# Optimization experiments

Hardware: AMD Instinct MI355X
Metric: run time of the kernel (lower is better)

## Reference

```python
import jax, jax.numpy as jnp
import numpy as np
import itertools
jax.config.update("jax_enable_x64", True)

ND, NQ, B = 4, 3, 256          # ndrives, nqubits, batch_size
D = 2 ** NQ                     # Hilbert-space dim = 8


def _pauli_basis(nq):
    I = np.eye(2, dtype=np.complex128)
    X = np.array([[0, 1], [1, 0]], dtype=np.complex128)
    Y = np.array([[0, -1j], [1j, 0]], dtype=np.complex128)
    Z = np.array([[1, 0], [0, -1]], dtype=np.complex128)
    mats = []
    for combo in itertools.product([I, X, Y, Z], repeat=nq):
        m = np.array([[1.0 + 0j]], dtype=np.complex128)
        for s in combo:
            m = np.kron(m, s)
        mats.append(m)
    return np.stack(mats)  # [4**nq, 2**nq, 2**nq], Hermitian


def setup_inputs() -> dict:
    key = jax.random.key(0)
    k1, k2, k3 = jax.random.split(key, 3)
    paulies = jnp.asarray(_pauli_basis(NQ))          # [64, 8, 8] complex128
    L = paulies.shape[0]
    x = jax.random.normal(k1, (B, ND), dtype=jnp.float64)
    # keras 'normal' initializer ~ stddev 0.05
    kernel = 0.05 * jax.random.normal(k2, (ND, L), dtype=jnp.float64)
    bias = 0.05 * jax.random.normal(k3, (L,), dtype=jnp.float64)
    return {"x": x, "kernel": kernel, "bias": bias, "paulies": paulies}


def _probs(pw_i, paulies):
    # pw_i: [L] real pauli weights for one sample
    H = jnp.tensordot(pw_i.astype(jnp.complex128), paulies, axes=[[0], [0]])  # [D, D]
    e, v = jnp.linalg.eigh(H)                      # Hermitian eigendecomp
    expe = jnp.exp(-1j * e)                        # [D]
    # amp_j = sum_s conj(v)[0,s] * exp(-i e_s) * v[j,s]  (evolution of |0>)
    amp = jnp.einsum('s,js->j', jnp.conj(v[0, :]) * expe, v)  # [D]
    return amp.real ** 2 + amp.imag ** 2           # P, [D] float64


def reference(x, kernel, bias, paulies):
    pw = x @ kernel + bias                         # [B, L]
    f = lambda p: _probs(p, paulies)
    P = jax.vmap(f)(pw)                            # [B, D]
    # per-sample Jacobian dP/d(pauli_weights): [B, D, L]
    g = jax.vmap(jax.jacrev(f))(pw)
    oneoverp = 1.0 / P                             # [B, D]
    # chain rule: pw = x @ kernel + bias  =>  dP/dkernel[i,p,j,k] = x[i,j] * g[i,p,k]
    p_k = jnp.einsum('ij,ipk->ipjk', x, g)         # [B, D, ND, L]
    I_k = jnp.einsum('ipjk,iplm,ip->ijklm', p_k, p_k, oneoverp)  # [B, ND, L, ND, L]
    I_b = jnp.einsum('ipj,ipk,ip->ijk', g, g, oneoverp)          # [B, L, L]
    return (I_k, I_b)
```

## Files before the change

### kernel.cpp

```cpp
#include <hip/hip_runtime.h>
#include <math.h>

typedef float f4_t __attribute__((ext_vector_type(4)));

#define NTERM 20
#define TROW  9
#define TMAT  (TROW * 8)

__device__ __forceinline__ double rdin(const void* p, int idx, bool isdbl) {
  return isdbl ? ((const double*)p)[idx] : (double)((const float*)p)[idx];
}

__global__ __launch_bounds__(256) void fi_all(
    const void* __restrict__ xv,
    const void* __restrict__ kv,
    const void* __restrict__ bv,
    float* __restrict__ out, int Bn)
{
  const int i    = blockIdx.x;
  const int t    = threadIdx.x;
  const int wv   = t >> 6;
  const int tl   = t & 63;
  const int swv  = i & 3;
  const bool solver = (wv == swv);

  __shared__ float  pw[64];
  __shared__ float2 Zl[8][8];
  __shared__ float  invfact[48];
  __shared__ float2 Tall[NTERM * TMAT];
  __shared__ float2 Rl[NTERM][8];
  __shared__ float2 Ql[8][8][8];
  __shared__ float  ampre[8], ampim[8], invPs[8];
  __shared__ __align__(16) float gk_km[64][8];
  __shared__ __align__(16) float hk_t[8][68];

  const bool isdbl =
      (__ballot(!(fabsf(((const float*)xv)[tl]) < 1e6f)) != 0ull);

  if (solver) {
    float acc = (float)rdin(bv, tl, isdbl);
    #pragma unroll
    for (int j = 0; j < 4; ++j)
      acc += (float)rdin(xv, i*4 + j, isdbl) * (float)rdin(kv, j*64 + tl, isdbl);
    pw[tl] = acc;
  } else if (wv == ((swv + 1) & 3) && tl < 48) {
    int n = tl;
    float f = 1.0f;
    for (int u = 2; u <= n; ++u) f *= __builtin_amdgcn_rcpf((float)u);
    invfact[n] = f;
  }
  __syncthreads();

  if (solver) {
    int r = tl >> 3, c = tl & 7;
    int m = r ^ c;
    float hre = 0.0f, him = 0.0f;
    for (int u = 0; u < 8; ++u) {
      int k = 0;
      float pr = 1.0f, pim = 0.0f;
      #pragma unroll
      for (int q = 0; q < 3; ++q) {
        int bit = 2 - q;
        int f  = (m >> bit) & 1;
        int ch = (u >> bit) & 1;
        int rb = (r >> bit) & 1;
        int d  = f ? (ch ? 2 : 1) : (ch ? 3 : 0);
        k = (k << 2) | d;
        if (d == 2) {
          float nr = rb ? -pim : pim;
          float ni = rb ?  pr  : -pr;
          pr = nr; pim = ni;
        } else if (d == 3 && rb) { pr = -pr; pim = -pim; }
      }
      float w = pw[k];
      hre += w * pr; him += w * pim;
    }
    Zl[r][c] = make_float2(him, -hre);
  }
  __syncthreads();

  if (solver) {
    const int r = tl >> 3, c = tl & 7;
    float2 Zrow[8];
    #pragma unroll
    for (int u = 0; u < 8; ++u) Zrow[u] = Zl[r][u];
    float Tre = (r == c) ? 1.0f : 0.0f;
    float Tim = 0.0f;
    Tall[r*TROW + c] = make_float2(Tre, Tim);
    #pragma unroll
    for (int j = 1; j < NTERM; ++j) {
      float cr[8], ci[8];
      #pragma unroll
      for (int u = 0; u < 8; ++u) {
        int srcl = (((u << 3) | c) << 2);
        cr[u] = __int_as_float(__builtin_amdgcn_ds_bpermute(srcl, __float_as_int(Tre)));
        ci[u] = __int_as_float(__builtin_amdgcn_ds_bpermute(srcl, __float_as_int(Tim)));
      }
      float nr = 0.0f, ni = 0.0f;
      #pragma unroll
      for (int u = 0; u < 8; ++u) {
        nr += Zrow[u].x*cr[u] - Zrow[u].y*ci[u];
        ni += Zrow[u].x*ci[u] + Zrow[u].y*cr[u];
      }
      Tre = nr; Tim = ni;
      Tall[j*TMAT + r*TROW + c] = make_float2(nr, ni);
    }
  }
  __syncthreads();

  if (t < NTERM * 8) {
    const int l = t >> 3, b = t & 7;
    float sr = 0.0f, si = 0.0f;
    for (int j = 0; j < NTERM; ++j) {
      float cf = invfact[j + l + 1];
      float2 a = Tall[j*TMAT + b*TROW];
      sr += cf * a.x; si += cf * a.y;
    }
    Rl[l][b] = make_float2(sr, si);
  }
  if (t >= 192 && t < 200) {
    const int b = t - 192;
    float ar = 0.0f, ai = 0.0f;
    for (int j = 0; j < NTERM; ++j) {
      float cf = invfact[j];
      float2 a = Tall[j*TMAT + b*TROW];
      ar += cf * a.x; ai += cf * a.y;
    }
    ampre[b] = ar; ampim[b] = ai;
    float P = ar*ar + ai*ai;
    invPs[b] = 1.0f / fmaxf(P, 1e-30f);
  }
  __syncthreads();

  {
    const int p  = t >> 5;
    const int a  = (t >> 2) & 7;
    const int b0 = (t & 3) << 1;
    float q0r = 0.f, q0i = 0.f, q1r = 0.f, q1i = 0.f;
    for (int l = 0; l < NTERM; ++l) {
      float2 T  = Tall[l*TMAT + p*TROW + a];
      f4_t  rp  = *(const f4_t*)&Rl[l][b0];
      q0r += T.x*rp.x - T.y*rp.y;  q0i += T.x*rp.y + T.y*rp.x;
      q1r += T.x*rp.z - T.y*rp.w;  q1i += T.x*rp.w + T.y*rp.z;
    }
    Ql[p][a][b0]   = make_float2(q0r, q0i);
    Ql[p][a][b0+1] = make_float2(q1r, q1i);
  }
  __syncthreads();

  {
    const int k  = t & 63;
    const int pg = t >> 6;
    const int p0 = pg << 1, p1 = p0 + 1;
    const int d0 = (k >> 4) & 3, d1 = (k >> 2) & 3, d2 = k & 3;
    const int m = ((((d0 == 1) | (d0 == 2)) ? 1 : 0) << 2)
                | ((((d1 == 1) | (d1 == 2)) ? 1 : 0) << 1)
                |  (((d2 == 1) | (d2 == 2)) ? 1 : 0);
    float S0r = 0.f, S0i = 0.f, S1r = 0.f, S1i = 0.f;
    #pragma unroll
    for (int a = 0; a < 8; ++a) {
      float pr = 1.0f, pim = 0.0f;
      const int dd[3] = {d0, d1, d2};
      #pragma unroll
      for (int q = 0; q < 3; ++q) {
        int rb = (a >> (2 - q)) & 1;
        int d = dd[q];
        if (d == 2) {
          float nr = rb ? -pim : pim;
          float ni = rb ?  pr  : -pr;
          pr = nr; pim = ni;
        } else if (d == 3 && rb) { pr = -pr; pim = -pim; }
      }
      const int b = a ^ m;
      float2 qa = Ql[p0][a][b];
      float2 qb = Ql[p1][a][b];
      S0r += pr*qa.x - pim*qa.y;  S0i += pr*qa.y + pim*qa.x;
      S1r += pr*qb.x - pim*qb.y;  S1i += pr*qb.y + pim*qb.x;
    }
    float g0 = 2.0f * (ampre[p0]*S0i - ampim[p0]*S0r);
    float g1 = 2.0f * (ampre[p1]*S1i - ampim[p1]*S1r);
    *(float2*)&gk_km[k][p0] = make_float2(g0, g1);
    hk_t[p0][k] = g0 * invPs[p0];
    hk_t[p1][k] = g1 * invPs[p1];
  }

  float sc[4];
  {
    float xl = (float)rdin(xv, i*4 + (tl >> 4), isdbl);
    #pragma unroll
    for (int jj = 0; jj < 4; ++jj)
      sc[jj] = xl * (float)rdin(xv, i*4 + jj, isdbl);
  }
  __syncthreads();

  const int m4 = (tl & 15) << 2;
  f4_t hv[8];
  #pragma unroll
  for (int p = 0; p < 8; ++p) hv[p] = *(const f4_t*)&hk_t[p][m4];

  {
    float* ok = out + (size_t)i * 65536;
    #pragma unroll
    for (int it = 0; it < 16; ++it) {
      const int k = it*4 + wv;
      const f4_t ga = *(const f4_t*)&gk_km[k][0];
      const f4_t gb = *(const f4_t*)&gk_km[k][4];
      f4_t acc = ga.x*hv[0] + ga.y*hv[1] + ga.z*hv[2] + ga.w*hv[3]
               + gb.x*hv[4] + gb.y*hv[5] + gb.z*hv[6] + gb.w*hv[7];
      #pragma unroll
      for (int jj = 0; jj < 4; ++jj) {
        f4_t vv = sc[jj] * acc;
        *(f4_t*)(ok + (size_t)jj*16384 + (size_t)k*256 + (size_t)tl*4) = vv;
      }
    }
  }

  {
    float* ob = out + (size_t)Bn * 65536 + (size_t)i * 4096;
    #pragma unroll
    for (int r = 0; r < 4; ++r) {
      const int k = r*16 + (t >> 4);
      const f4_t ga = *(const f4_t*)&gk_km[k][0];
      const f4_t gb = *(const f4_t*)&gk_km[k][4];
      f4_t acc = ga.x*hv[0] + ga.y*hv[1] + ga.z*hv[2] + ga.w*hv[3]
               + gb.x*hv[4] + gb.y*hv[5] + gb.z*hv[6] + gb.w*hv[7];
      *(f4_t*)(ob + (size_t)r*1024 + (size_t)t*4) = acc;
    }
  }
}

extern "C" void kernel_launch(void* const* d_in, const int* in_sizes, int n_in,
                              void* d_out, int out_size, void* d_ws, size_t ws_size,
                              hipStream_t stream) {
  (void)n_in; (void)d_ws; (void)ws_size; (void)out_size;
  int Bn = in_sizes[0] / 4;
  fi_all<<<Bn, 256, 0, stream>>>(d_in[0], d_in[1], d_in[2], (float*)d_out, Bn);
}
```

Measured before the change: 93.06 us.

## Split matrix power series across all four wavefronts using repeated squaring

Instead of one solver wavefront computing Z^1..Z^19 serially, every wavefront builds pw and Z redundantly in registers via cross-lane permutes. Each wavefront then jumps to its own starting power (Z^0, Z^5, Z^10, Z^15) by squaring and computes five consecutive powers. This removes two barriers and shortens the serial chain of matrix products. The inverse-factorial table becomes a constant array. Redundant work grows across wavefronts, and squaring changes float rounding slightly.

Result: faster. 91.23 us, median of 2 (-2.0%).

```diff
diff --git a/kernel.cpp b/kernel.cpp
--- a/kernel.cpp
+++ b/kernel.cpp
@@ -7,8 +7,57 @@
 #define TROW  9
 #define TMAT  (TROW * 8)
 
+__device__ const float INVFACT[48] = {
+  1.0f, 1.0f, 5.0e-1f, 1.66666666666667e-1f, 4.16666666666667e-2f,
+  8.33333333333333e-3f, 1.38888888888889e-3f, 1.98412698412698e-4f,
+  2.48015873015873e-5f, 2.75573192239859e-6f, 2.75573192239859e-7f,
+  2.50521083854417e-8f, 2.08767569878681e-9f, 1.60590438368216e-10f,
+  1.14707455977297e-11f, 7.64716373181982e-13f, 4.77947733238738e-14f,
+  2.81145725434552e-15f, 1.56192069685862e-16f, 8.22063524662433e-18f,
+  4.11031762331216e-19f, 1.95729410633913e-20f, 8.89679139245057e-22f,
+  3.86817017063068e-23f, 1.61173757109612e-24f, 6.44695028438447e-26f,
+  2.47959626322480e-27f, 9.18368986379555e-29f, 3.27988923706984e-30f,
+  1.13099628864477e-31f, 3.76998762881591e-33f, 1.21612504155352e-34f,
+  3.80039075485474e-36f, 1.15163356207720e-37f, 3.38715753552116e-39f,
+  0.f, 0.f, 0.f, 0.f, 0.f, 0.f, 0.f, 0.f, 0.f, 0.f, 0.f, 0.f, 0.f
+};
+
 __device__ __forceinline__ double rdin(const void* p, int idx, bool isdbl) {
   return isdbl ? ((const double*)p)[idx] : (double)((const float*)p)[idx];
+}
+
+__device__ __forceinline__ float bpf(int srcl, float v) {
+  return __int_as_float(__builtin_amdgcn_ds_bpermute(srcl, __float_as_int(v)));
+}
+
+__device__ __forceinline__ void gmul(float& Cr, float& Ci,
+                                     float Ar, float Ai, float Br, float Bi,
+                                     int r, int c) {
+  float nr = 0.f, ni = 0.f;
+  #pragma unroll
+  for (int u = 0; u < 8; ++u) {
+    int sa = ((r << 3) | u) << 2;
+    int sb = ((u << 3) | c) << 2;
+    float ar = bpf(sa, Ar), ai = bpf(sa, Ai);
+    float br = bpf(sb, Br), bi = bpf(sb, Bi);
+    nr += ar*br - ai*bi;
+    ni += ar*bi + ai*br;
+  }
+  Cr = nr; Ci = ni;
+}
+
+__device__ __forceinline__ void zmul(float& Cr, float& Ci,
+                                     float Br, float Bi,
+                                     const float2* Zrow, int c) {
+  float nr = 0.f, ni = 0.f;
+  #pragma unroll
+  for (int u = 0; u < 8; ++u) {
+    int sb = ((u << 3) | c) << 2;
+    float br = bpf(sb, Br), bi = bpf(sb, Bi);
+    nr += Zrow[u].x*br - Zrow[u].y*bi;
+    ni += Zrow[u].x*bi + Zrow[u].y*br;
+  }
+  Cr = nr; Ci = ni;
 }
 
 __global__ __launch_bounds__(256) void fi_all(
@@ -21,12 +70,7 @@
   const int t    = threadIdx.x;
   const int wv   = t >> 6;
   const int tl   = t & 63;
-  const int swv  = i & 3;
-  const bool solver = (wv == swv);
-
-  __shared__ float  pw[64];
-  __shared__ float2 Zl[8][8];
-  __shared__ float  invfact[48];
+
   __shared__ float2 Tall[NTERM * TMAT];
   __shared__ float2 Rl[NTERM][8];
   __shared__ float2 Ql[8][8][8];
@@ -37,27 +81,19 @@
   const bool isdbl =
       (__ballot(!(fabsf(((const float*)xv)[tl]) < 1e6f)) != 0ull);
 
-  if (solver) {
-    float acc = (float)rdin(bv, tl, isdbl);
-    #pragma unroll
-    for (int j = 0; j < 4; ++j)
-      acc += (float)rdin(xv, i*4 + j, isdbl) * (float)rdin(kv, j*64 + tl, isdbl);
-    pw[tl] = acc;
-  } else if (wv == ((swv + 1) & 3) && tl < 48) {
-    int n = tl;
-    float f = 1.0f;
-    for (int u = 2; u <= n; ++u) f *= __builtin_amdgcn_rcpf((float)u);
-    invfact[n] = f;
-  }
-  __syncthreads();
-
-  if (solver) {
-    int r = tl >> 3, c = tl & 7;
+  float pwv = (float)rdin(bv, tl, isdbl);
+  #pragma unroll
+  for (int j = 0; j < 4; ++j)
+    pwv += (float)rdin(xv, i*4 + j, isdbl) * (float)rdin(kv, j*64 + tl, isdbl);
+
+  const int r = tl >> 3, c = tl & 7;
+  float Zre, Zim;
+  {
     int m = r ^ c;
-    float hre = 0.0f, him = 0.0f;
+    float hre = 0.f, him = 0.f;
+    #pragma unroll
     for (int u = 0; u < 8; ++u) {
-      int k = 0;
-      float pr = 1.0f, pim = 0.0f;
+      int k = 0; float pr = 1.f, pim = 0.f;
       #pragma unroll
       for (int q = 0; q < 3; ++q) {
         int bit = 2 - q;
@@ -72,38 +108,48 @@
           pr = nr; pim = ni;
         } else if (d == 3 && rb) { pr = -pr; pim = -pim; }
       }
-      float w = pw[k];
+      float w = bpf(k << 2, pwv);
       hre += w * pr; him += w * pim;
     }
-    Zl[r][c] = make_float2(him, -hre);
-  }
-  __syncthreads();
-
-  if (solver) {
-    const int r = tl >> 3, c = tl & 7;
-    float2 Zrow[8];
-    #pragma unroll
-    for (int u = 0; u < 8; ++u) Zrow[u] = Zl[r][u];
-    float Tre = (r == c) ? 1.0f : 0.0f;
-    float Tim = 0.0f;
-    Tall[r*TROW + c] = make_float2(Tre, Tim);
-    #pragma unroll
-    for (int j = 1; j < NTERM; ++j) {
-      float cr[8], ci[8];
-      #pragma unroll
-      for (int u = 0; u < 8; ++u) {
-        int srcl = (((u << 3) | c) << 2);
-        cr[u] = __int_as_float(__builtin_amdgcn_ds_bpermute(srcl, __float_as_int(Tre)));
-        ci[u] = __int_as_float(__builtin_amdgcn_ds_bpermute(srcl, __float_as_int(Tim)));
-      }
-      float nr = 0.0f, ni = 0.0f;
-      #pragma unroll
-      for (int u = 0; u < 8; ++u) {
-        nr += Zrow[u].x*cr[u] - Zrow[u].y*ci[u];
-        ni += Zrow[u].x*ci[u] + Zrow[u].y*cr[u];
-      }
-      Tre = nr; Tim = ni;
-      Tall[j*TMAT + r*TROW + c] = make_float2(nr, ni);
+    Zre = him; Zim = -hre;
+  }
+
+  float2 Zrow[8];
+  #pragma unroll
+  for (int u = 0; u < 8; ++u) {
+    int s = ((r << 3) | u) << 2;
+    Zrow[u] = make_float2(bpf(s, Zre), bpf(s, Zim));
+  }
+
+  float Z2r, Z2i; zmul(Z2r, Z2i, Zre, Zim, Zrow, c);
+  if (wv == 0) {
+    Tall[0*TMAT + r*TROW + c] = make_float2((r == c) ? 1.f : 0.f, 0.f);
+    Tall[1*TMAT + r*TROW + c] = make_float2(Zre, Zim);
+    Tall[2*TMAT + r*TROW + c] = make_float2(Z2r, Z2i);
+    float cr_ = Z2r, ci_ = Z2i;
+    #pragma unroll
+    for (int s = 3; s < 5; ++s) {
+      float nr_, ni_; zmul(nr_, ni_, cr_, ci_, Zrow, c);
+      cr_ = nr_; ci_ = ni_;
+      Tall[s*TMAT + r*TROW + c] = make_float2(cr_, ci_);
+    }
+  } else {
+    float Z4r, Z4i; gmul(Z4r, Z4i, Z2r, Z2i, Z2r, Z2i, r, c);
+    float Z5r, Z5i; zmul(Z5r, Z5i, Z4r, Z4i, Zrow, c);
+    float Cr_, Ci_;
+    if (wv == 1) { Cr_ = Z5r; Ci_ = Z5i; }
+    else {
+      float Z10r, Z10i; gmul(Z10r, Z10i, Z5r, Z5i, Z5r, Z5i, r, c);
+      if (wv == 2) { Cr_ = Z10r; Ci_ = Z10i; }
+      else         { gmul(Cr_, Ci_, Z10r, Z10i, Z5r, Z5i, r, c); }
+    }
+    const int base = wv * 5;
+    Tall[base*TMAT + r*TROW + c] = make_float2(Cr_, Ci_);
+    #pragma unroll
+    for (int s = 1; s < 5; ++s) {
+      float nr_, ni_; zmul(nr_, ni_, Cr_, Ci_, Zrow, c);
+      Cr_ = nr_; Ci_ = ni_;
+      Tall[(base + s)*TMAT + r*TROW + c] = make_float2(Cr_, Ci_);
     }
   }
   __syncthreads();
@@ -111,8 +157,9 @@
   if (t < NTERM * 8) {
     const int l = t >> 3, b = t & 7;
     float sr = 0.0f, si = 0.0f;
+    #pragma unroll
     for (int j = 0; j < NTERM; ++j) {
-      float cf = invfact[j + l + 1];
+      float cf = INVFACT[j + l + 1];
       float2 a = Tall[j*TMAT + b*TROW];
       sr += cf * a.x; si += cf * a.y;
     }
@@ -121,8 +168,9 @@
   if (t >= 192 && t < 200) {
     const int b = t - 192;
     float ar = 0.0f, ai = 0.0f;
+    #pragma unroll
     for (int j = 0; j < NTERM; ++j) {
-      float cf = invfact[j];
+      float cf = INVFACT[j];
       float2 a = Tall[j*TMAT + b*TROW];
       ar += cf * a.x; ai += cf * a.y;
     }
@@ -137,6 +185,7 @@
     const int a  = (t >> 2) & 7;
     const int b0 = (t & 3) << 1;
     float q0r = 0.f, q0i = 0.f, q1r = 0.f, q1i = 0.f;
+    #pragma unroll
     for (int l = 0; l < NTERM; ++l) {
       float2 T  = Tall[l*TMAT + p*TROW + a];
       f4_t  rp  = *(const f4_t*)&Rl[l][b0];
@@ -218,13 +267,13 @@
   {
     float* ob = out + (size_t)Bn * 65536 + (size_t)i * 4096;
     #pragma unroll
-    for (int r = 0; r < 4; ++r) {
-      const int k = r*16 + (t >> 4);
+    for (int rr = 0; rr < 4; ++rr) {
+      const int k = rr*16 + (t >> 4);
       const f4_t ga = *(const f4_t*)&gk_km[k][0];
       const f4_t gb = *(const f4_t*)&gk_km[k][4];
       f4_t acc = ga.x*hv[0] + ga.y*hv[1] + ga.z*hv[2] + ga.w*hv[3]
                + gb.x*hv[4] + gb.y*hv[5] + gb.z*hv[6] + gb.w*hv[7];
-      *(f4_t*)(ob + (size_t)r*1024 + (size_t)t*4) = acc;
+      *(f4_t*)(ob + (size_t)rr*1024 + (size_t)t*4) = acc;
     }
   }
 }
```
